# Kernel optimization log

Measured on AMD Instinct MI355X. Metric: run time of the kernel, lower is better.

Reference implementation:

```python
import jax, jax.numpy as jnp
import numpy as np

T, Hs, Ws, MAX_D = 8, 14, 14, 3
D_WIN = 2 * MAX_D + 1  # 7


def l2norm(x, axis, eps=1e-12):
    # matches torch F.normalize
    n = jnp.sqrt(jnp.sum(x * x, axis=axis, keepdims=True))
    return x / jnp.maximum(n, eps)


def correlation(q, k):
    # q, k: (B, d, H, W). FlowNet-style cost volume with max_displacement=3,
    # kernel_size=1, zero padding at borders. Output (B, 49, H*W).
    B, d, H, W = q.shape
    kp = jnp.pad(k, ((0, 0), (0, 0), (MAX_D, MAX_D), (MAX_D, MAX_D)))
    planes = [jnp.sum(q * kp[:, :, u:u + H, v:v + W], axis=1)
              for u in range(D_WIN) for v in range(D_WIN)]
    return jnp.stack(planes, axis=1).reshape(B, D_WIN * D_WIN, H * W)


def setup_inputs() -> dict:
    key = jax.random.key(0)
    ks = jax.random.split(key, 5)
    B, N, C = 16, T * Hs * Ws, 768
    x = jax.random.normal(ks[0], (B, N, C), dtype=jnp.float32)
    w_qkv = jax.random.normal(ks[1], (C, 3 * C), dtype=jnp.float32) * (1.0 / np.sqrt(C))
    w_proj = jax.random.normal(ks[2], (C, C), dtype=jnp.float32) * (1.0 / np.sqrt(C))
    b_proj = jnp.zeros((C,), dtype=jnp.float32)
    pos_embed = jax.random.normal(ks[3], (1, D_WIN * D_WIN, Hs * Ws), dtype=jnp.float32) * 0.02
    return {"x": x, "w_qkv": w_qkv, "w_proj": w_proj, "b_proj": b_proj,
            "pos_embed": pos_embed}


def reference(x, w_qkv, w_proj, b_proj, pos_embed):
    B, N, C = x.shape
    nh = 8
    hd = C // nh
    HW = Hs * Ws
    # qkv: (3, B, nh, N, hd)
    qkv = (x @ w_qkv).reshape(B, N, 3, nh, hd).transpose(2, 0, 3, 1, 4)
    q, k, v = qkv[0], qkv[1], qkv[2]
    # 'b n (t h w) d -> (b n) t d h w'
    q = q.reshape(B * nh, T, Hs, Ws, hd).transpose(0, 1, 4, 2, 3)
    k = k.reshape(B * nh, T, Hs, Ws, hd).transpose(0, 1, 4, 2, 3)
    # v: '(b n t) (h w) d'
    v = v.reshape(B * nh * T, HW, hd)
    # temporal shift: k_postfix[t] = k[t+1], last repeated
    k_post = jnp.concatenate([k[:, 1:], k[:, -1:]], axis=1)
    qp = l2norm(q.reshape(B * nh * T, hd, Hs, Ws), axis=1)
    kp = l2norm(k_post.reshape(B * nh * T, hd, Hs, Ws), axis=1)
    # cost volume (BhT, 49, HW) + positional embedding
    corr = correlation(qp, kp) + pos_embed
    # motion branch: corr^T @ corr -> (BhT, HW, HW)
    motion_attn = jax.nn.softmax(jnp.einsum('bun,bum->bnm', corr, corr), axis=-1)
    motion_x = jnp.einsum('bnm,bmd->bnd', motion_attn, v)
    # appearance branch
    qf = qp.reshape(B * nh * T, hd, HW).transpose(0, 2, 1)  # (BhT, HW, hd)
    kf = kp.reshape(B * nh * T, hd, HW)                      # (BhT, hd, HW)
    app_attn = jax.nn.softmax(jnp.einsum('bnd,bdm->bnm', qf, kf), axis=-1)
    app_x = jnp.einsum('bnm,bmd->bnd', app_attn, v)

    def merge(y):
        # '(b n t) (h w) d -> b n (t h w) d' then 'b h n d -> b n (h d)'
        y = y.reshape(B, nh, T * HW, hd).transpose(0, 2, 1, 3)
        return y.reshape(B, N, C)

    out = 0.5 * merge(app_x) + 0.5 * merge(motion_x)
    return out @ w_proj + b_proj
```

## Files before the change

### kernel.cpp

```cpp
#include <hip/hip_runtime.h>
#include <hip/hip_bf16.h>

namespace {

constexpr int T = 8, HW = 196;
constexpr int C = 768, NH = 8, HD = 96;
constexpr int NTOK = 1568;
constexpr int BHT = 1024;
constexpr int C3 = 2304;
constexpr int CHW = HD * HW;
constexpr int NROWS = 25088;
constexpr int NT = 13;
constexpr int KW = 104;
constexpr int VW2 = 212;
constexpr int UW = 72;

using bf16 = __hip_bfloat16;
typedef __attribute__((ext_vector_type(8))) short short8v;
typedef __attribute__((ext_vector_type(4))) float f32x4;

__device__ __forceinline__ float b2f(bf16 h) { return __bfloat162float(h); }
__device__ __forceinline__ bf16 f2b(float f) { return __float2bfloat16(f); }
__device__ __forceinline__ float u2f(ushort u) {
  union { ushort u[2]; float f; } x; x.u[0] = 0; x.u[1] = u; return x.f;
}
__device__ __forceinline__ ushort b2u(bf16 h) { union { bf16 b; ushort u; } x; x.b = h; return x.u; }
__device__ __forceinline__ uint pk2(float lo, float hi) {
  return ((uint)b2u(f2b(hi)) << 16) | (uint)b2u(f2b(lo));
}
__device__ __forceinline__ void gload_lds16(const bf16* g, bf16* l) {
  __builtin_amdgcn_global_load_lds(
      (const __attribute__((address_space(1))) unsigned int*)g,
      (__attribute__((address_space(3))) unsigned int*)l, 16, 0, 0);
}

__global__ __launch_bounds__(256) void conv_to_bf16(
    const float* __restrict__ X, bf16* __restrict__ Y, int n8) {
  const int i = blockIdx.x * 256 + threadIdx.x;
  if (i >= n8) return;
  const float4 a = ((const float4*)X)[i * 2];
  const float4 b = ((const float4*)X)[i * 2 + 1];
  uint4 o;
  o.x = pk2(a.x, a.y); o.y = pk2(a.z, a.w);
  o.z = pk2(b.x, b.y); o.w = pk2(b.z, b.w);
  ((uint4*)Y)[i] = o;
}

__global__ __launch_bounds__(256) void transpose_to_bf16(
    const float* __restrict__ W, bf16* __restrict__ Wt, int rows, int cols) {
  __shared__ __align__(16) bf16 Lt[64][72];
  const int r0 = blockIdx.y * 64, c0 = blockIdx.x * 64;
  const int tid = threadIdx.x;
  const int r = tid >> 2, q = (tid & 3) * 16;
  const float* src = W + (size_t)(r0 + r) * cols + c0 + q;
#pragma unroll
  for (int i = 0; i < 16; i += 4) {
    const float4 v = *(const float4*)(src + i);
    Lt[q + i + 0][r] = f2b(v.x);
    Lt[q + i + 1][r] = f2b(v.y);
    Lt[q + i + 2][r] = f2b(v.z);
    Lt[q + i + 3][r] = f2b(v.w);
  }
  __syncthreads();
  const int c = tid >> 2, kc = (tid & 3) * 16;
  uint4* dst = (uint4*)(Wt + (size_t)(c0 + c) * rows + r0 + kc);
  const uint4* srcl = (const uint4*)(&Lt[c][kc]);
  dst[0] = srcl[0];
  dst[1] = srcl[1];
}

__device__ __forceinline__ void gemm128_core(
    const bf16* __restrict__ A, const bf16* __restrict__ Bt,
    int rt, int ct, bf16* As, bf16* Bs, f32x4 acc[4][4]) {
  const int tid = threadIdx.x;
  const int w = tid >> 6, lane = tid & 63;
  const int lr = lane & 15, lg = lane >> 4;
  const int wr = w >> 1, wc = w & 1;
  const int crow = (lane >> 3);
  const int cole = (lane & 7) * 8;
#pragma unroll
  for (int i = 0; i < 4; ++i)
#pragma unroll
    for (int j = 0; j < 4; ++j) acc[i][j] = (f32x4){0.f, 0.f, 0.f, 0.f};

  for (int kt = 0; kt < 12; ++kt) {
    const int k0 = kt * 64;
    __syncthreads();
#pragma unroll
    for (int i = 0; i < 4; ++i) {
      const int chunk = w * 4 + i;
      const int row = chunk * 8 + crow;
      gload_lds16(A + (size_t)(rt + row) * 768 + k0 + cole, As + chunk * 512);
      gload_lds16(Bt + (size_t)(ct + row) * 768 + k0 + cole, Bs + chunk * 512);
    }
    __syncthreads();
#pragma unroll
    for (int kc = 0; kc < 2; ++kc) {
      short8v xa[4], wb[4];
#pragma unroll
      for (int f = 0; f < 4; ++f) {
        xa[f] = *(const short8v*)(As + (wr * 64 + f * 16 + lr) * 64 + kc * 32 + lg * 8);
        wb[f] = *(const short8v*)(Bs + (wc * 64 + f * 16 + lr) * 64 + kc * 32 + lg * 8);
      }
#pragma unroll
      for (int cj = 0; cj < 4; ++cj)
#pragma unroll
        for (int ri = 0; ri < 4; ++ri)
          acc[cj][ri] = __builtin_amdgcn_mfma_f32_16x16x32_bf16(wb[cj], xa[ri], acc[cj][ri], 0, 0, 0);
    }
  }
}

__global__ __launch_bounds__(256) void gemm_qkv_mfma(
    const bf16* __restrict__ A, const bf16* __restrict__ Bt,
    bf16* __restrict__ Qo, bf16* __restrict__ Ko, bf16* __restrict__ Vo) {
  __shared__ __align__(16) bf16 As[128 * 64];
  __shared__ __align__(16) bf16 Bs[128 * 64];
  const int id = blockIdx.x;
  const int sw = (id & 7) * 441 + (id >> 3);
  const int cti = sw % 18, rti = sw / 18;
  const int ct = cti * 128, rt = rti * 128;
  const int tid = threadIdx.x;
  const int w = tid >> 6, lane = tid & 63;
  const int lr = lane & 15, lg = lane >> 4;
  const int wr = w >> 1, wc = w & 1;

  f32x4 acc[4][4];
  gemm128_core(A, Bt, rt, ct, As, Bs, acc);

  const int s = cti / 6;
#pragma unroll
  for (int ri = 0; ri < 4; ++ri) {
    const int row = rt + wr * 64 + ri * 16 + lr;
    const int b_ = row / NTOK, n = row % NTOK;
    const int t = n / HW, hw = n % HW;
#pragma unroll
    for (int cj = 0; cj < 4; ++cj) {
      const int colb = ct + wc * 64 + cj * 16 + lg * 4;
      const int rem = colb - s * C;
      const int head = rem / HD, chb = rem - head * HD;
      const int bh = b_ * NH + head;
      if (s == 0) {
        uint2 pk;
        pk.x = pk2(acc[cj][ri][0], acc[cj][ri][1]);
        pk.y = pk2(acc[cj][ri][2], acc[cj][ri][3]);
        *(uint2*)(Qo + (size_t)(bh * T + t) * CHW + hw * HD + chb) = pk;
      } else if (s == 1) {
        uint2 pk;
        pk.x = pk2(acc[cj][ri][0], acc[cj][ri][1]);
        pk.y = pk2(acc[cj][ri][2], acc[cj][ri][3]);
        if (t >= 1)
          *(uint2*)(Ko + (size_t)(bh * T + t - 1) * CHW + hw * HD + chb) = pk;
        if (t == T - 1)
          *(uint2*)(Ko + (size_t)(bh * T + t) * CHW + hw * HD + chb) = pk;
      } else {
#pragma unroll
        for (int j = 0; j < 4; ++j)
          Vo[(size_t)(bh * T + t) * CHW + (chb + j) * HW + hw] = f2b(acc[cj][ri][j]);
      }
    }
  }
}

__global__ __launch_bounds__(256) void gemm_proj_mfma(
    const bf16* __restrict__ A, const bf16* __restrict__ Bt,
    const float* __restrict__ bias, float* __restrict__ out) {
  __shared__ __align__(16) bf16 As[128 * 64];
  __shared__ __align__(16) bf16 Bs[128 * 64];
  const int id = blockIdx.x;
  const int sw = (id & 7) * 147 + (id >> 3);
  const int cti = sw % 6, rti = sw / 6;
  const int ct = cti * 128, rt = rti * 128;
  const int tid = threadIdx.x;
  const int w = tid >> 6, lane = tid & 63;
  const int lr = lane & 15, lg = lane >> 4;
  const int wr = w >> 1, wc = w & 1;

  f32x4 acc[4][4];
  gemm128_core(A, Bt, rt, ct, As, Bs, acc);

#pragma unroll
  for (int ri = 0; ri < 4; ++ri) {
    const int row = rt + wr * 64 + ri * 16 + lr;
#pragma unroll
    for (int cj = 0; cj < 4; ++cj) {
      const int colb = ct + wc * 64 + cj * 16 + lg * 4;
      const float4 bv = *(const float4*)(bias + colb);
      float4 o;
      o.x = acc[cj][ri][0] + bv.x;
      o.y = acc[cj][ri][1] + bv.y;
      o.z = acc[cj][ri][2] + bv.z;
      o.w = acc[cj][ri][3] + bv.w;
      *(float4*)(out + (size_t)row * C + colb) = o;
    }
  }
}

__global__ __launch_bounds__(1024, 1) void fused_attn(
    const bf16* __restrict__ Qg, const bf16* __restrict__ Kg,
    const bf16* __restrict__ Vg, const float* __restrict__ pos,
    bf16* __restrict__ merged) {
  __shared__ __align__(16) bf16 Klds[208 * KW];
  __shared__ __align__(16) bf16 Vt[96 * VW2];
  __shared__ __align__(16) bf16 corrT[208 * UW];
  __shared__ float invQ[208];
  const int bt = blockIdx.x;
  const int tid = threadIdx.x;
  const int w = tid >> 6, lane = tid & 63;
  const int lr = lane & 15, lg = lane >> 4;
  const size_t gbase = (size_t)bt * CHW;

  {
    const uint4* kg = (const uint4*)(Kg + gbase);
    uint4* kl = (uint4*)Klds;
    for (int i = tid; i < 196 * 12; i += 1024) { const int r = i / 12, g = i - r * 12; kl[r * 13 + g] = kg[i]; }
    const uint4 z4 = make_uint4(0u, 0u, 0u, 0u);
    for (int i = tid; i < 12 * 13; i += 1024) { const int r = 196 + i / 13, g = i % 13; kl[r * 13 + g] = z4; }
    const uint* vg = (const uint*)(Vg + gbase);
    uint* vl = (uint*)Vt;
    for (int i = tid; i < 96 * 98; i += 1024) { const int c = i / 98, g = i - c * 98; vl[c * 106 + g] = vg[i]; }
    for (int i = tid; i < 96 * 8; i += 1024)  { const int c = i / 8, g = 98 + (i & 7); vl[c * 106 + g] = 0u; }
    uint* ct32 = (uint*)corrT;
    for (int i = tid; i < 208 * 36; i += 1024) {
      const int n = i % 208, up = i / 208;
      const int u0 = 2 * up, u1 = u0 + 1;
      const float p0 = (n < 196 && u0 < 49) ? pos[u0 * 196 + n] : 0.f;
      const float p1 = (n < 196 && u1 < 49) ? pos[u1 * 196 + n] : 0.f;
      ct32[n * 36 + up] = pk2(p0, p1);
    }
    if (tid < 208) {
      float s = 0.f;
      if (tid < 196) {
        const uint* qr = (const uint*)(Qg + gbase + (size_t)tid * HD);
#pragma unroll
        for (int g = 0; g < 48; ++g) {
          const uint pk = qr[g];
          const float a = u2f((ushort)(pk & 0xffff));
          const float b = u2f((ushort)(pk >> 16));
          s += a * a + b * b;
        }
      }
      invQ[tid] = 1.f / fmaxf(sqrtf(s), 1e-12f);
    }
  }
  __syncthreads();
  if (tid < 208) {
    uint* rowp = (uint*)(Klds + tid * KW);
    float s = 0.f;
#pragma unroll
    for (int g = 0; g < 48; ++g) {
      const uint pk = rowp[g];
      const float a = u2f((ushort)(pk & 0xffff));
      const float b = u2f((ushort)(pk >> 16));
      s += a * a + b * b;
    }
    const float inv = 1.f / fmaxf(sqrtf(s), 1e-12f);
#pragma unroll
    for (int g = 0; g < 48; ++g) {
      const uint pk = rowp[g];
      rowp[g] = pk2(u2f((ushort)(pk & 0xffff)) * inv, u2f((ushort)(pk >> 16)) * inv);
    }
  }
  __syncthreads();

  const int b_ = bt >> 6, head = (bt >> 3) & 7, tt = bt & 7;
  union PW { short8v v; uint u[4]; };
  const int rt = w;
  f32x4 pacc[6];
#pragma unroll
  for (int ct = 0; ct < 6; ++ct) pacc[ct] = (f32x4){0.f, 0.f, 0.f, 0.f};

  if (rt < NT) {
    const int rq = (rt * 16 + lr > 195) ? 195 : rt * 16 + lr;
    short8v qf[3];
#pragma unroll
    for (int kc = 0; kc < 3; ++kc)
      qf[kc] = *(const short8v*)(Qg + gbase + (size_t)rq * HD + kc * 32 + lg * 8);
    f32x4 sacc[NT];
#pragma unroll
    for (int mt = 0; mt < NT; ++mt) sacc[mt] = (f32x4){0.f, 0.f, 0.f, 0.f};
    __builtin_amdgcn_s_setprio(1);
#pragma unroll
    for (int kc = 0; kc < 3; ++kc)
#pragma unroll
      for (int mt = 0; mt < NT; ++mt) {
        const short8v kf = *(const short8v*)&Klds[(mt * 16 + lr) * KW + kc * 32 + lg * 8];
        sacc[mt] = __builtin_amdgcn_mfma_f32_16x16x32_bf16(kf, qf[kc], sacc[mt], 0, 0, 0);
      }
    __builtin_amdgcn_s_setprio(0);
    const float iq = invQ[rq];
#pragma unroll
    for (int mt = 0; mt < NT; ++mt) {
      sacc[mt][0] *= iq; sacc[mt][1] *= iq; sacc[mt][2] *= iq; sacc[mt][3] *= iq;
    }
    const int rowg = rt * 16 + lr;
    if (rowg < 196) {
      const int h = rowg / 14, wq = rowg - (rowg / 14) * 14;
      int h2 = 0, w2 = lg * 4;
#pragma unroll
      for (int mt = 0; mt < NT; ++mt) {
        int hh = h2, ww = w2;
#pragma unroll
        for (int r = 0; r < 4; ++r) {
          if (mt < 12 || lg * 4 + r < 4) {
            const int dh = hh - h + 3, dw = ww - wq + 3;
            if (((unsigned)dh < 7u) && ((unsigned)dw < 7u)) {
              bf16* cp = &corrT[rowg * UW + dh * 7 + dw];
              *cp = f2b(b2f(*cp) + sacc[mt][r]);
            }
          }
          if (++ww == 14) { ww = 0; ++hh; }
        }
        w2 += 2; h2 += 1; if (w2 >= 14) { w2 -= 14; h2 += 1; }
      }
    }
    float m0 = -1e30f, m1 = -1e30f, m2 = -1e30f, m3 = -1e30f;
#pragma unroll
    for (int mt = 0; mt < 12; ++mt) {
      m0 = fmaxf(m0, sacc[mt][0]); m1 = fmaxf(m1, sacc[mt][1]);
      m2 = fmaxf(m2, sacc[mt][2]); m3 = fmaxf(m3, sacc[mt][3]);
    }
    if (lg == 0) {
      m0 = fmaxf(m0, sacc[12][0]); m1 = fmaxf(m1, sacc[12][1]);
      m2 = fmaxf(m2, sacc[12][2]); m3 = fmaxf(m3, sacc[12][3]);
    }
    float mx = fmaxf(fmaxf(m0, m1), fmaxf(m2, m3));
    mx = fmaxf(mx, __shfl_xor(mx, 16));
    mx = fmaxf(mx, __shfl_xor(mx, 32));
    float s0 = 0.f, s1 = 0.f, s2 = 0.f, s3 = 0.f;
#pragma unroll
    for (int mt = 0; mt < NT; ++mt) {
      const bool dead = (mt == 12) && (lg != 0);
      const float e0 = dead ? 0.f : __expf(sacc[mt][0] - mx);
      const float e1 = dead ? 0.f : __expf(sacc[mt][1] - mx);
      const float e2 = dead ? 0.f : __expf(sacc[mt][2] - mx);
      const float e3 = dead ? 0.f : __expf(sacc[mt][3] - mx);
      sacc[mt][0] = e0; sacc[mt][1] = e1; sacc[mt][2] = e2; sacc[mt][3] = e3;
      s0 += e0; s1 += e1; s2 += e2; s3 += e3;
    }
    float s = (s0 + s1) + (s2 + s3);
    s += __shfl_xor(s, 16); s += __shfl_xor(s, 32);
    const float sc = 0.5f / s;
    PW pf[7];
#pragma unroll
    for (int kb = 0; kb < 7; ++kb) {
      pf[kb].u[0] = pk2(sacc[2 * kb][0] * sc, sacc[2 * kb][1] * sc);
      pf[kb].u[1] = pk2(sacc[2 * kb][2] * sc, sacc[2 * kb][3] * sc);
      if (kb < 6) {
        pf[kb].u[2] = pk2(sacc[2 * kb + 1][0] * sc, sacc[2 * kb + 1][1] * sc);
        pf[kb].u[3] = pk2(sacc[2 * kb + 1][2] * sc, sacc[2 * kb + 1][3] * sc);
      } else { pf[kb].u[2] = 0u; pf[kb].u[3] = 0u; }
    }
    __builtin_amdgcn_s_setprio(1);
#pragma unroll
    for (int ct = 0; ct < 6; ++ct) {
      const int c = ct * 16 + lr;
#pragma unroll
      for (int kb = 0; kb < 7; ++kb) {
        const uint2 lo = *(const uint2*)&Vt[c * VW2 + (2 * kb) * 16 + lg * 4];
        const uint2 hi = (kb < 6) ? *(const uint2*)&Vt[c * VW2 + (2 * kb + 1) * 16 + lg * 4] : lo;
        PW vf; vf.u[0] = lo.x; vf.u[1] = lo.y; vf.u[2] = hi.x; vf.u[3] = hi.y;
        pacc[ct] = __builtin_amdgcn_mfma_f32_16x16x32_bf16(pf[kb].v, vf.v, pacc[ct], 0, 0, 0);
      }
    }
    __builtin_amdgcn_s_setprio(0);
  }
  __syncthreads();

  if (rt < NT) {
    short8v cq[2];
#pragma unroll
    for (int kc = 0; kc < 2; ++kc)
      cq[kc] = *(const short8v*)&corrT[(rt * 16 + lr) * UW + kc * 32 + lg * 8];
    f32x4 macc[NT];
#pragma unroll
    for (int mt = 0; mt < NT; ++mt) macc[mt] = (f32x4){0.f, 0.f, 0.f, 0.f};
    __builtin_amdgcn_s_setprio(1);
#pragma unroll
    for (int kc = 0; kc < 2; ++kc)
#pragma unroll
      for (int mt = 0; mt < NT; ++mt) {
        const short8v ca = *(const short8v*)&corrT[(mt * 16 + lr) * UW + kc * 32 + lg * 8];
        macc[mt] = __builtin_amdgcn_mfma_f32_16x16x32_bf16(ca, cq[kc], macc[mt], 0, 0, 0);
      }
    __builtin_amdgcn_s_setprio(0);
    float m0 = -1e30f, m1 = -1e30f, m2 = -1e30f, m3 = -1e30f;
#pragma unroll
    for (int mt = 0; mt < 12; ++mt) {
      m0 = fmaxf(m0, macc[mt][0]); m1 = fmaxf(m1, macc[mt][1]);
      m2 = fmaxf(m2, macc[mt][2]); m3 = fmaxf(m3, macc[mt][3]);
    }
    if (lg == 0) {
      m0 = fmaxf(m0, macc[12][0]); m1 = fmaxf(m1, macc[12][1]);
      m2 = fmaxf(m2, macc[12][2]); m3 = fmaxf(m3, macc[12][3]);
    }
    float mx = fmaxf(fmaxf(m0, m1), fmaxf(m2, m3));
    mx = fmaxf(mx, __shfl_xor(mx, 16));
    mx = fmaxf(mx, __shfl_xor(mx, 32));
    float s0 = 0.f, s1 = 0.f, s2 = 0.f, s3 = 0.f;
#pragma unroll
    for (int mt = 0; mt < NT; ++mt) {
      const bool dead = (mt == 12) && (lg != 0);
      const float e0 = dead ? 0.f : __expf(macc[mt][0] - mx);
      const float e1 = dead ? 0.f : __expf(macc[mt][1] - mx);
      const float e2 = dead ? 0.f : __expf(macc[mt][2] - mx);
      const float e3 = dead ? 0.f : __expf(macc[mt][3] - mx);
      macc[mt][0] = e0; macc[mt][1] = e1; macc[mt][2] = e2; macc[mt][3] = e3;
      s0 += e0; s1 += e1; s2 += e2; s3 += e3;
    }
    float s = (s0 + s1) + (s2 + s3);
    s += __shfl_xor(s, 16); s += __shfl_xor(s, 32);
    const float sc = 0.5f / s;
    PW pf[7];
#pragma unroll
    for (int kb = 0; kb < 7; ++kb) {
      pf[kb].u[0] = pk2(macc[2 * kb][0] * sc, macc[2 * kb][1] * sc);
      pf[kb].u[1] = pk2(macc[2 * kb][2] * sc, macc[2 * kb][3] * sc);
      if (kb < 6) {
        pf[kb].u[2] = pk2(macc[2 * kb + 1][0] * sc, macc[2 * kb + 1][1] * sc);
        pf[kb].u[3] = pk2(macc[2 * kb + 1][2] * sc, macc[2 * kb + 1][3] * sc);
      } else { pf[kb].u[2] = 0u; pf[kb].u[3] = 0u; }
    }
    __builtin_amdgcn_s_setprio(1);
#pragma unroll
    for (int ct = 0; ct < 6; ++ct) {
      const int c = ct * 16 + lr;
#pragma unroll
      for (int kb = 0; kb < 7; ++kb) {
        const uint2 lo = *(const uint2*)&Vt[c * VW2 + (2 * kb) * 16 + lg * 4];
        const uint2 hi = (kb < 6) ? *(const uint2*)&Vt[c * VW2 + (2 * kb + 1) * 16 + lg * 4] : lo;
        PW vf; vf.u[0] = lo.x; vf.u[1] = lo.y; vf.u[2] = hi.x; vf.u[3] = hi.y;
        pacc[ct] = __builtin_amdgcn_mfma_f32_16x16x32_bf16(pf[kb].v, vf.v, pacc[ct], 0, 0, 0);
      }
    }
    __builtin_amdgcn_s_setprio(0);
#pragma unroll
    for (int r = 0; r < 4; ++r) {
      const int rowq = rt * 16 + lg * 4 + r;
      if (rowq < 196) {
        const size_t ob = ((size_t)(b_ * NTOK + tt * HW + rowq)) * C + head * HD;
#pragma unroll
        for (int ct = 0; ct < 6; ++ct)
          merged[ob + ct * 16 + lr] = f2b(pacc[ct][r]);
      }
    }
  }
}

}

extern "C" void kernel_launch(void* const* d_in, const int* in_sizes, int n_in,
                              void* d_out, int out_size, void* d_ws, size_t ws_size,
                              hipStream_t stream) {
  (void)in_sizes; (void)n_in; (void)out_size; (void)ws_size;
  const float* x      = (const float*)d_in[0];
  const float* w_qkv  = (const float*)d_in[1];
  const float* w_proj = (const float*)d_in[2];
  const float* b_proj = (const float*)d_in[3];
  const float* pos    = (const float*)d_in[4];
  float* out = (float*)d_out;

  char* p = (char*)d_ws;
  bf16* Qb = (bf16*)p;      p += (size_t)BHT * CHW * sizeof(bf16);
  bf16* Kb = (bf16*)p;      p += (size_t)BHT * CHW * sizeof(bf16);
  bf16* Vb = (bf16*)p;      p += (size_t)BHT * CHW * sizeof(bf16);
  bf16* xbm = (bf16*)p;     p += (size_t)NROWS * C * sizeof(bf16);
  bf16* wqkvT = (bf16*)p;   p += (size_t)C3 * C * sizeof(bf16);
  bf16* wprojT = (bf16*)p;  p += (size_t)C * C * sizeof(bf16);

  conv_to_bf16<<<(NROWS * C / 8 + 255) / 256, 256, 0, stream>>>(x, xbm, NROWS * C / 8);
  transpose_to_bf16<<<dim3(C3 / 64, C / 64), 256, 0, stream>>>(w_qkv, wqkvT, C, C3);
  transpose_to_bf16<<<dim3(C / 64, C / 64), 256, 0, stream>>>(w_proj, wprojT, C, C);
  gemm_qkv_mfma<<<3528, 256, 0, stream>>>(xbm, wqkvT, Qb, Kb, Vb);
  fused_attn<<<BHT, 1024, 0, stream>>>(Qb, Kb, Vb, pos, xbm );
  gemm_proj_mfma<<<1176, 256, 0, stream>>>(xbm, wprojT, b_proj, out);
}
```

Baseline: 344.0 us.

## Double-buffer LDS tiles in shared MFMA GEMM core to overlap loads

Converts the shared 128x128 GEMM core used by the QKV and projection kernels from single-buffered LDS staging to double buffering. The next K tile is issued with global_load_lds into the alternate buffer before the MFMAs on the current tile run, leaving one barrier per iteration instead of two. This is meant to hide global-to-LDS latency behind compute. In exchange LDS use per block doubles to 64KB, which may lower occupancy.

```diff
diff --git a/kernel.cpp b/kernel.cpp
--- a/kernel.cpp
+++ b/kernel.cpp
@@ -14,6 +14,7 @@
 constexpr int KW = 104;
 constexpr int VW2 = 212;
 constexpr int UW = 72;
+constexpr int TSZ = 128 * 64;
 
 using bf16 = __hip_bfloat16;
 typedef __attribute__((ext_vector_type(8))) short short8v;
@@ -83,24 +84,31 @@
 #pragma unroll
     for (int j = 0; j < 4; ++j) acc[i][j] = (f32x4){0.f, 0.f, 0.f, 0.f};
 
+#define STAGE_T(kt, dA, dB)                                                   \
+  {                                                                           \
+    const int k0s = (kt) * 64;                                                \
+    _Pragma("unroll") for (int i = 0; i < 4; ++i) {                           \
+      const int chunk = w * 4 + i;                                            \
+      const int row = chunk * 8 + crow;                                       \
+      gload_lds16(A + (size_t)(rt + row) * 768 + k0s + cole, (dA) + chunk * 512); \
+      gload_lds16(Bt + (size_t)(ct + row) * 768 + k0s + cole, (dB) + chunk * 512); \
+    }                                                                         \
+  }
+
+  STAGE_T(0, As, Bs);
+  __syncthreads();
+#pragma unroll
   for (int kt = 0; kt < 12; ++kt) {
-    const int k0 = kt * 64;
-    __syncthreads();
-#pragma unroll
-    for (int i = 0; i < 4; ++i) {
-      const int chunk = w * 4 + i;
-      const int row = chunk * 8 + crow;
-      gload_lds16(A + (size_t)(rt + row) * 768 + k0 + cole, As + chunk * 512);
-      gload_lds16(Bt + (size_t)(ct + row) * 768 + k0 + cole, Bs + chunk * 512);
-    }
-    __syncthreads();
+    const int cur = (kt & 1) * TSZ;
+    const int nxt = ((kt + 1) & 1) * TSZ;
+    if (kt + 1 < 12) STAGE_T(kt + 1, As + nxt, Bs + nxt);
 #pragma unroll
     for (int kc = 0; kc < 2; ++kc) {
       short8v xa[4], wb[4];
 #pragma unroll
       for (int f = 0; f < 4; ++f) {
-        xa[f] = *(const short8v*)(As + (wr * 64 + f * 16 + lr) * 64 + kc * 32 + lg * 8);
-        wb[f] = *(const short8v*)(Bs + (wc * 64 + f * 16 + lr) * 64 + kc * 32 + lg * 8);
+        xa[f] = *(const short8v*)(As + cur + (wr * 64 + f * 16 + lr) * 64 + kc * 32 + lg * 8);
+        wb[f] = *(const short8v*)(Bs + cur + (wc * 64 + f * 16 + lr) * 64 + kc * 32 + lg * 8);
       }
 #pragma unroll
       for (int cj = 0; cj < 4; ++cj)
@@ -108,14 +116,16 @@
         for (int ri = 0; ri < 4; ++ri)
           acc[cj][ri] = __builtin_amdgcn_mfma_f32_16x16x32_bf16(wb[cj], xa[ri], acc[cj][ri], 0, 0, 0);
     }
-  }
+    __syncthreads();
+  }
+#undef STAGE_T
 }
 
 __global__ __launch_bounds__(256) void gemm_qkv_mfma(
     const bf16* __restrict__ A, const bf16* __restrict__ Bt,
     bf16* __restrict__ Qo, bf16* __restrict__ Ko, bf16* __restrict__ Vo) {
-  __shared__ __align__(16) bf16 As[128 * 64];
-  __shared__ __align__(16) bf16 Bs[128 * 64];
+  __shared__ __align__(16) bf16 As[2 * TSZ];
+  __shared__ __align__(16) bf16 Bs[2 * TSZ];
   const int id = blockIdx.x;
   const int sw = (id & 7) * 441 + (id >> 3);
   const int cti = sw % 18, rti = sw / 18;
@@ -165,8 +175,8 @@
 __global__ __launch_bounds__(256) void gemm_proj_mfma(
     const bf16* __restrict__ A, const bf16* __restrict__ Bt,
     const float* __restrict__ bias, float* __restrict__ out) {
-  __shared__ __align__(16) bf16 As[128 * 64];
-  __shared__ __align__(16) bf16 Bs[128 * 64];
+  __shared__ __align__(16) bf16 As[2 * TSZ];
+  __shared__ __align__(16) bf16 Bs[2 * TSZ];
   const int id = blockIdx.x;
   const int sw = (id & 7) * 147 + (id >> 3);
   const int cti = sw % 6, rti = sw / 6;
```

Measured after the change: 348.9 us. About the same (+1.4%).
